# Kernel optimization log

Hardware: AMD Instinct MI355X
Metric: run time of the kernel (lower is better)

## Reference

```python
import jax, jax.numpy as jnp
import numpy as np

B, P, H = 32768, 128, 64

def setup_inputs() -> dict:
    key = jax.random.key(0)
    ks = jax.random.split(key, 6)
    planet_xy = jax.random.normal(ks[0], (B, P, 2), dtype=jnp.float32)
    planet_m = jax.random.uniform(ks[1], (P,), dtype=jnp.float32)
    ast_xy = jax.random.normal(ks[2], (B, 2), dtype=jnp.float32)
    W1 = jax.random.normal(ks[3], (4, H), dtype=jnp.float32) * 0.5
    b1 = jnp.zeros((H,), dtype=jnp.float32)
    W2 = jax.random.normal(ks[4], (H, H), dtype=jnp.float32) * 0.125
    b2 = jnp.zeros((H,), dtype=jnp.float32)
    return {"planet_xy": planet_xy, "planet_m": planet_m, "ast_xy": ast_xy,
            "W1": W1, "b1": b1, "W2": W2, "b2": b2}

def reference(planet_xy, planet_m, ast_xy, W1, b1, W2, b2):
    # d: (B, P, 2) broadcast difference planet - asteroid
    d = planet_xy - ast_xy[:, None, :]
    dist2 = jnp.sum(d * d, axis=-1) + 1e-6            # (B, P)
    invdist = 1.0 / jnp.sqrt(dist2)                   # (B, P)
    m = jnp.broadcast_to(planet_m[None, :], dist2.shape)  # (B, P)
    feats = jnp.concatenate([d, invdist[..., None], m[..., None]], axis=-1)  # (B, P, 4)
    h = jax.nn.relu(jnp.einsum('bpf,fh->bph', feats, W1) + b1)  # (B, P, H)
    msg = jax.nn.relu(jnp.einsum('bph,hk->bpk', h, W2) + b2)    # (B, P, H)
    return msg.sum(axis=1)                             # (B, H)
```

## Files before the change

### kernel.cpp

```cpp
#include <hip/hip_runtime.h>
#include <hip/hip_fp16.h>

#define NP    128
#define NH    64
#define LDH   72
#define ITERS 4
#define WPB   4

typedef __attribute__((ext_vector_type(8))) _Float16 f16x8;
typedef __attribute__((ext_vector_type(4))) _Float16 f16x4;
typedef __attribute__((ext_vector_type(2))) __fp16  hf16x2;
typedef __attribute__((ext_vector_type(4))) float f32x4;
typedef __attribute__((ext_vector_type(2))) float f32x2;

union FragK32 { f16x8 v; unsigned int u[4]; };
union FragK16 { f16x4 v; unsigned int u[2]; };

__device__ __forceinline__ unsigned int pack_pkrtz(float a, float b) {
    hf16x2 t = __builtin_amdgcn_cvt_pkrtz(a, b);
    return __builtin_bit_cast(unsigned int, t);
}

__device__ __forceinline__ unsigned int relu2_pk(unsigned int u) {
    hf16x2 h = __builtin_bit_cast(hf16x2, u);
    h = __builtin_elementwise_max(h, (hf16x2)(__fp16)0.f);
    return __builtin_bit_cast(unsigned int, h);
}

__global__ void __launch_bounds__(256, 2) gnn_wave(
    const float* __restrict__ planet_xy,
    const float* __restrict__ planet_m,
    const float* __restrict__ ast_xy,
    const float* __restrict__ W1,
    const float* __restrict__ b1,
    const float* __restrict__ W2,
    const float* __restrict__ b2,
    float* __restrict__ out)
{
    __shared__ alignas(16) unsigned short slab[WPB][2][16 * LDH];

    const int tid  = threadIdx.x;
    const int wv   = tid >> 6;
    const int lane = tid & 63;
    const int q    = lane >> 4;
    const int lm   = lane & 15;
    const bool q0  = (q == 0);
    const bool q1  = (q == 1);

    FragK16 w1f[4];
    #pragma unroll
    for (int mt = 0; mt < 4; mt++) {
        const int m = 16 * mt + lm;
        float wa = W1[0 * NH + m], wb = W1[1 * NH + m];
        float wc = W1[2 * NH + m], wd = W1[3 * NH + m];
        float be = b1[m];
        w1f[mt].u[0] = q0 ? pack_pkrtz(wa, wb) : (q1 ? pack_pkrtz(be, 0.f) : 0u);
        w1f[mt].u[1] = q0 ? pack_pkrtz(wc, wd) : 0u;
    }

    FragK32 w2f[2][4];
    #pragma unroll
    for (int kk = 0; kk < 2; kk++)
        #pragma unroll
        for (int np = 0; np < 4; np++)
            #pragma unroll
            for (int jp = 0; jp < 4; jp++) {
                float r0 = W2[(32 * kk + 8 * q + 2 * jp + 0) * NH + 16 * np + lm];
                float r1 = W2[(32 * kk + 8 * q + 2 * jp + 1) * NH + 16 * np + lm];
                w2f[kk][np].u[jp] = pack_pkrtz(r0, r1);
            }

    f32x4 b2f[4];
    #pragma unroll
    for (int np = 0; np < 4; np++) {
        float v = b2[16 * np + lm];
        b2f[np] = (f32x4){v, v, v, v};
    }

    float pmv[8];
    #pragma unroll
    for (int i = 0; i < 8; i++)
        pmv[i] = planet_m[16 * i + lm];

    const unsigned int bf0_const = q1 ? pack_pkrtz(1.f, 0.f) : 0u;

    const f32x4 zf = (f32x4){0.f, 0.f, 0.f, 0.f};
    int b = (blockIdx.x * WPB + wv) * ITERS;

    for (int it = 0; it < ITERS; ++it, ++b) {
        const float2 axy = *(const float2*)&ast_xy[2 * b];
        float2 pxy[8];
        #pragma unroll
        for (int i = 0; i < 8; i++)
            pxy[i] = *(const float2*)&planet_xy[((size_t)b * NP + 16 * i + lm) * 2];

        f32x2 sum2[4];
        #pragma unroll
        for (int np = 0; np < 4; np++)
            sum2[np] = (f32x2){0.f, 0.f};

        {
            float dx = pxy[0].x - axy.x, dy = pxy[0].y - axy.y;
            float inv = __builtin_amdgcn_rsqf(fmaf(dx, dx, fmaf(dy, dy, 1e-6f)));
            FragK16 bf;
            bf.u[0] = q0 ? pack_pkrtz(dx, dy)      : bf0_const;
            bf.u[1] = q0 ? pack_pkrtz(inv, pmv[0]) : 0u;
            #pragma unroll
            for (int mt = 0; mt < 4; mt++) {
                f32x4 c = __builtin_amdgcn_mfma_f32_16x16x16f16(w1f[mt].v, bf.v, zf, 0, 0, 0);
                unsigned int d0 = relu2_pk(pack_pkrtz(c[0], c[1]));
                unsigned int d1 = relu2_pk(pack_pkrtz(c[2], c[3]));
                *(uint2*)&slab[wv][0][lm * LDH + 4 * q + 16 * mt] = make_uint2(d0, d1);
            }
        }

        #pragma unroll
        for (int mi = 0; mi < 8; ++mi) {
            const int buf = mi & 1;
            f16x8 a0 = *(const f16x8*)&slab[wv][buf][lm * LDH + 0  + 8 * q];
            f16x8 a1 = *(const f16x8*)&slab[wv][buf][lm * LDH + 32 + 8 * q];

            if (mi < 7) {
                float dx = pxy[mi + 1].x - axy.x, dy = pxy[mi + 1].y - axy.y;
                float inv = __builtin_amdgcn_rsqf(fmaf(dx, dx, fmaf(dy, dy, 1e-6f)));
                FragK16 bf;
                bf.u[0] = q0 ? pack_pkrtz(dx, dy)           : bf0_const;
                bf.u[1] = q0 ? pack_pkrtz(inv, pmv[mi + 1]) : 0u;
                #pragma unroll
                for (int mt = 0; mt < 4; mt++) {
                    f32x4 c = __builtin_amdgcn_mfma_f32_16x16x16f16(w1f[mt].v, bf.v, zf, 0, 0, 0);
                    unsigned int d0 = relu2_pk(pack_pkrtz(c[0], c[1]));
                    unsigned int d1 = relu2_pk(pack_pkrtz(c[2], c[3]));
                    *(uint2*)&slab[wv][buf ^ 1][lm * LDH + 4 * q + 16 * mt] = make_uint2(d0, d1);
                }
            }

            #pragma unroll
            for (int np = 0; np < 4; np++) {
                f32x4 acc = __builtin_amdgcn_mfma_f32_16x16x32_f16(a0, w2f[0][np].v, b2f[np], 0, 0, 0);
                acc = __builtin_amdgcn_mfma_f32_16x16x32_f16(a1, w2f[1][np].v, acc, 0, 0, 0);
                float m0 = fmaxf(acc[0], 0.f), m1 = fmaxf(acc[1], 0.f);
                float m2 = fmaxf(acc[2], 0.f), m3 = fmaxf(acc[3], 0.f);
                sum2[np] += (f32x2){m0, m1};
                sum2[np] += (f32x2){m2, m3};
            }
        }

        #pragma unroll
        for (int np = 0; np < 4; np++) {
            float s = sum2[np].x + sum2[np].y;
            s += __shfl_xor(s, 16, 64);
            s += __shfl_xor(s, 32, 64);
            if (q0) out[(size_t)b * NH + 16 * np + lm] = s;
        }
    }
}

extern "C" void kernel_launch(void* const* d_in, const int* in_sizes, int n_in,
                              void* d_out, int out_size, void* d_ws, size_t ws_size,
                              hipStream_t stream) {
    const float* planet_xy = (const float*)d_in[0];
    const float* planet_m  = (const float*)d_in[1];
    const float* ast_xy    = (const float*)d_in[2];
    const float* W1        = (const float*)d_in[3];
    const float* b1        = (const float*)d_in[4];
    const float* W2        = (const float*)d_in[5];
    const float* b2        = (const float*)d_in[6];
    float* outp            = (float*)d_out;

    const int B = in_sizes[2] / 2;
    const int batches_per_block = WPB * ITERS;
    const int grid = (B + batches_per_block - 1) / batches_per_block;

    gnn_wave<<<grid, 256, 0, stream>>>(planet_xy, planet_m, ast_xy, W1, b1, W2, b2, outp);
}
```

Measured before the change: 150.0 us.

## Keep layer-1 activations in registers by computing transposed layer-2 MFMA

The second layer is reformulated as W2^T times h, so the 16x16x16 MFMA output of layer 1 serves directly as the B operand of the layer-2 MFMAs. This removes the per-tile LDS round trip and double-buffered slab for hidden activations. The reduction over planets now happens along lanes, so it goes through a small padded LDS transpose per batch item instead of shuffles. The cost is 16 smaller MFMAs per tile instead of 8 K32 ones, plus an extra LDS write/read for the final reduction.

After: 139.7 us. -6.9%, faster.

```diff
diff --git a/kernel.cpp b/kernel.cpp
--- a/kernel.cpp
+++ b/kernel.cpp
@@ -3,17 +3,14 @@
 
 #define NP    128
 #define NH    64
-#define LDH   72
+#define RST   18
 #define ITERS 4
 #define WPB   4
 
-typedef __attribute__((ext_vector_type(8))) _Float16 f16x8;
 typedef __attribute__((ext_vector_type(4))) _Float16 f16x4;
 typedef __attribute__((ext_vector_type(2))) __fp16  hf16x2;
 typedef __attribute__((ext_vector_type(4))) float f32x4;
-typedef __attribute__((ext_vector_type(2))) float f32x2;
 
-union FragK32 { f16x8 v; unsigned int u[4]; };
 union FragK16 { f16x4 v; unsigned int u[2]; };
 
 __device__ __forceinline__ unsigned int pack_pkrtz(float a, float b) {
@@ -37,7 +34,7 @@
     const float* __restrict__ b2,
     float* __restrict__ out)
 {
-    __shared__ alignas(16) unsigned short slab[WPB][2][16 * LDH];
+    __shared__ float rsum[WPB][64 * RST];
 
     const int tid  = threadIdx.x;
     const int wv   = tid >> 6;
@@ -58,24 +55,25 @@
         w1f[mt].u[1] = q0 ? pack_pkrtz(wc, wd) : 0u;
     }
 
-    FragK32 w2f[2][4];
+    FragK16 w2tf[4][4];
     #pragma unroll
-    for (int kk = 0; kk < 2; kk++)
+    for (int np = 0; np < 4; np++)
         #pragma unroll
-        for (int np = 0; np < 4; np++)
-            #pragma unroll
-            for (int jp = 0; jp < 4; jp++) {
-                float r0 = W2[(32 * kk + 8 * q + 2 * jp + 0) * NH + 16 * np + lm];
-                float r1 = W2[(32 * kk + 8 * q + 2 * jp + 1) * NH + 16 * np + lm];
-                w2f[kk][np].u[jp] = pack_pkrtz(r0, r1);
-            }
+        for (int mt = 0; mt < 4; mt++) {
+            const int kbase = 16 * mt + 4 * q;
+            const int n = 16 * np + lm;
+            float r0 = W2[(kbase + 0) * NH + n];
+            float r1 = W2[(kbase + 1) * NH + n];
+            float r2 = W2[(kbase + 2) * NH + n];
+            float r3 = W2[(kbase + 3) * NH + n];
+            w2tf[np][mt].u[0] = pack_pkrtz(r0, r1);
+            w2tf[np][mt].u[1] = pack_pkrtz(r2, r3);
+        }
 
     f32x4 b2f[4];
     #pragma unroll
-    for (int np = 0; np < 4; np++) {
-        float v = b2[16 * np + lm];
-        b2f[np] = (f32x4){v, v, v, v};
-    }
+    for (int np = 0; np < 4; np++)
+        b2f[np] = *(const f32x4*)&b2[16 * np + 4 * q];
 
     float pmv[8];
     #pragma unroll
@@ -83,8 +81,8 @@
         pmv[i] = planet_m[16 * i + lm];
 
     const unsigned int bf0_const = q1 ? pack_pkrtz(1.f, 0.f) : 0u;
+    const f32x4 zf = (f32x4){0.f, 0.f, 0.f, 0.f};
 
-    const f32x4 zf = (f32x4){0.f, 0.f, 0.f, 0.f};
     int b = (blockIdx.x * WPB + wv) * ITERS;
 
     for (int it = 0; it < ITERS; ++it, ++b) {
@@ -94,65 +92,50 @@
         for (int i = 0; i < 8; i++)
             pxy[i] = *(const float2*)&planet_xy[((size_t)b * NP + 16 * i + lm) * 2];
 
-        f32x2 sum2[4];
+        f32x4 sums[4];
         #pragma unroll
         for (int np = 0; np < 4; np++)
-            sum2[np] = (f32x2){0.f, 0.f};
+            sums[np] = zf;
 
-        {
-            float dx = pxy[0].x - axy.x, dy = pxy[0].y - axy.y;
+        #pragma unroll
+        for (int mi = 0; mi < 8; ++mi) {
+            float dx = pxy[mi].x - axy.x, dy = pxy[mi].y - axy.y;
             float inv = __builtin_amdgcn_rsqf(fmaf(dx, dx, fmaf(dy, dy, 1e-6f)));
             FragK16 bf;
-            bf.u[0] = q0 ? pack_pkrtz(dx, dy)      : bf0_const;
-            bf.u[1] = q0 ? pack_pkrtz(inv, pmv[0]) : 0u;
+            bf.u[0] = q0 ? pack_pkrtz(dx, dy)        : bf0_const;
+            bf.u[1] = q0 ? pack_pkrtz(inv, pmv[mi])  : 0u;
+
+            FragK16 hb[4];
             #pragma unroll
             for (int mt = 0; mt < 4; mt++) {
                 f32x4 c = __builtin_amdgcn_mfma_f32_16x16x16f16(w1f[mt].v, bf.v, zf, 0, 0, 0);
-                unsigned int d0 = relu2_pk(pack_pkrtz(c[0], c[1]));
-                unsigned int d1 = relu2_pk(pack_pkrtz(c[2], c[3]));
-                *(uint2*)&slab[wv][0][lm * LDH + 4 * q + 16 * mt] = make_uint2(d0, d1);
+                hb[mt].u[0] = relu2_pk(pack_pkrtz(c[0], c[1]));
+                hb[mt].u[1] = relu2_pk(pack_pkrtz(c[2], c[3]));
+            }
+
+            #pragma unroll
+            for (int np = 0; np < 4; np++) {
+                f32x4 acc = b2f[np];
+                #pragma unroll
+                for (int mt = 0; mt < 4; mt++)
+                    acc = __builtin_amdgcn_mfma_f32_16x16x16f16(w2tf[np][mt].v, hb[mt].v, acc, 0, 0, 0);
+                sums[np] += __builtin_elementwise_max(acc, zf);
             }
         }
 
         #pragma unroll
-        for (int mi = 0; mi < 8; ++mi) {
-            const int buf = mi & 1;
-            f16x8 a0 = *(const f16x8*)&slab[wv][buf][lm * LDH + 0  + 8 * q];
-            f16x8 a1 = *(const f16x8*)&slab[wv][buf][lm * LDH + 32 + 8 * q];
+        for (int np = 0; np < 4; np++)
+            #pragma unroll
+            for (int r = 0; r < 4; r++)
+                rsum[wv][(16 * np + 4 * q + r) * RST + lm] = sums[np][r];
 
-            if (mi < 7) {
-                float dx = pxy[mi + 1].x - axy.x, dy = pxy[mi + 1].y - axy.y;
-                float inv = __builtin_amdgcn_rsqf(fmaf(dx, dx, fmaf(dy, dy, 1e-6f)));
-                FragK16 bf;
-                bf.u[0] = q0 ? pack_pkrtz(dx, dy)           : bf0_const;
-                bf.u[1] = q0 ? pack_pkrtz(inv, pmv[mi + 1]) : 0u;
-                #pragma unroll
-                for (int mt = 0; mt < 4; mt++) {
-                    f32x4 c = __builtin_amdgcn_mfma_f32_16x16x16f16(w1f[mt].v, bf.v, zf, 0, 0, 0);
-                    unsigned int d0 = relu2_pk(pack_pkrtz(c[0], c[1]));
-                    unsigned int d1 = relu2_pk(pack_pkrtz(c[2], c[3]));
-                    *(uint2*)&slab[wv][buf ^ 1][lm * LDH + 4 * q + 16 * mt] = make_uint2(d0, d1);
-                }
-            }
-
-            #pragma unroll
-            for (int np = 0; np < 4; np++) {
-                f32x4 acc = __builtin_amdgcn_mfma_f32_16x16x32_f16(a0, w2f[0][np].v, b2f[np], 0, 0, 0);
-                acc = __builtin_amdgcn_mfma_f32_16x16x32_f16(a1, w2f[1][np].v, acc, 0, 0, 0);
-                float m0 = fmaxf(acc[0], 0.f), m1 = fmaxf(acc[1], 0.f);
-                float m2 = fmaxf(acc[2], 0.f), m3 = fmaxf(acc[3], 0.f);
-                sum2[np] += (f32x2){m0, m1};
-                sum2[np] += (f32x2){m2, m3};
-            }
+        float tot = 0.f;
+        #pragma unroll
+        for (int i = 0; i < 8; i++) {
+            float2 v = *(const float2*)&rsum[wv][lane * RST + 2 * i];
+            tot += v.x + v.y;
         }
-
-        #pragma unroll
-        for (int np = 0; np < 4; np++) {
-            float s = sum2[np].x + sum2[np].y;
-            s += __shfl_xor(s, 16, 64);
-            s += __shfl_xor(s, 32, 64);
-            if (q0) out[(size_t)b * NH + 16 * np + lm] = s;
-        }
+        out[(size_t)b * NH + lane] = tot;
     }
 }
 
```
